# Kernel optimization log

Hardware: AMD Instinct MI355X
Metric: run time of the kernel (lower is better)

## Reference

```python
import jax, jax.numpy as jnp
import numpy as np
from jax.scipy.linalg import solve_triangular

REG = 1e-6  # reg_covar added to covariance diagonal
LOG2PI = float(np.log(2.0 * np.pi))
RESP_EPS = 10.0 * float(np.finfo(np.float32).eps)


def _log_gauss(X, means, covs):
    # X: [N,D], means: [K,D], covs: [K,D,D] -> per-sample per-component log N(x|mu_k, Sigma_k): [N,K]
    K, D = means.shape
    eye = jnp.eye(D, dtype=X.dtype)
    chol = jnp.linalg.cholesky(covs + REG * eye)                      # [K,D,D]
    diff = X[None, :, :] - means[:, None, :]                          # [K,N,D]
    sol = jax.vmap(lambda L, d: solve_triangular(L, d.T, lower=True))(chol, diff)  # [K,D,N]
    maha = jnp.sum(sol * sol, axis=1)                                 # [K,N]
    logdet = jnp.sum(jnp.log(jnp.diagonal(chol, axis1=1, axis2=2)), axis=1)  # [K] = 0.5*log|Sigma|
    return (-0.5 * (D * LOG2PI + maha) - logdet[:, None]).T           # [N,K]


def _em_step(X, weights, means, covs):
    N, D = X.shape
    # E-step: responsibilities via stable logsumexp
    lp = _log_gauss(X, means, covs) + jnp.log(weights)[None, :]       # [N,K]
    log_norm = jax.scipy.special.logsumexp(lp, axis=1)                # [N]
    resp = jnp.exp(lp - log_norm[:, None])                            # [N,K]
    # M-step (MLE)
    nk = resp.sum(axis=0) + RESP_EPS                                  # [K]
    new_w = nk / N
    new_means = (resp.T @ X) / nk[:, None]                            # [K,D]
    diff = X[None, :, :] - new_means[:, None, :]                      # [K,N,D]
    new_covs = jnp.einsum('kn,knd,kne->kde', resp.T, diff, diff) / nk[:, None, None]
    new_covs = new_covs + REG * jnp.eye(D, dtype=X.dtype)
    return new_w, new_means, new_covs


def reference(X, weights, means, covariances, n_iter):
    # Normalize provided weights (uniform init in the torch module)
    w0 = weights / jnp.sum(weights)

    def step(carry, _):
        w, m, c = carry
        return _em_step(X, w, m, c), None

    (w, m, c), _ = jax.lax.scan(step, (w0, means, covariances), xs=None, length=n_iter)
    # Final per-sample log-likelihood under the fitted mixture (lower bound)
    lp = _log_gauss(X, m, c) + jnp.log(w)[None, :]
    return jax.scipy.special.logsumexp(lp, axis=1)                    # [N]


def setup_inputs() -> dict:
    key = jax.random.key(0)
    kx, km = jax.random.split(key)
    N, D, K = 100000, 32, 16
    X = jax.random.normal(kx, (N, D), dtype=jnp.float32)
    weights = jnp.ones((K,), dtype=jnp.float32) / K
    means = jax.random.normal(km, (K, D), dtype=jnp.float32)
    covariances = jnp.tile(jnp.eye(D, dtype=jnp.float32)[None], (K, 1, 1))
    return {"X": X, "weights": weights, "means": means, "covariances": covariances, "n_iter": 5}
```

## Files before the change

kernel.cpp:

```cpp
#include <hip/hip_runtime.h>
#include <math.h>

#define REGC 1e-6f
#define LOG2PI 1.83787706640934534f
#define RESP_EPS 1.1920929e-6f

#define NSLOT 64
#define SSTR 568

typedef __attribute__((ext_vector_type(8))) short short8;
typedef __attribute__((ext_vector_type(4))) float f32x4;
typedef unsigned short ushort_t;
typedef unsigned int uint_t;

__device__ __forceinline__ ushort_t f2bf(float x) {
    uint_t u = __float_as_uint(x);
    uint_t r = (u + 0x7fffu + ((u >> 16) & 1u)) >> 16;
    return (ushort_t)r;
}
__device__ __forceinline__ float bf2f(ushort_t h) {
    return __uint_as_float(((uint_t)h) << 16);
}
__device__ __forceinline__ f32x4 shx4(f32x4 v, int m) {
    f32x4 r;
#pragma unroll
    for (int i = 0; i < 4; ++i) r[i] = __shfl_xor(v[i], m);
    return r;
}
__device__ __forceinline__ f32x4 sel4(bool s, f32x4 b, f32x4 a) {
    f32x4 r;
#pragma unroll
    for (int i = 0; i < 4; ++i) r[i] = s ? b[i] : a[i];
    return r;
}
__device__ __forceinline__ short8 pack_rx(const float* r8, const short8 bh, float& row) {
    uint_t u[8];
#pragma unroll
    for (int jj = 0; jj < 8; ++jj) {
        float av = r8[jj] * bf2f((ushort_t)bh[jj]);
        row += av;
        u[jj] = __float_as_uint(av) + 0x8000u;
    }
    short8 out;
    uint_t* o = (uint_t*)&out;
    o[0] = __builtin_amdgcn_perm(u[1], u[0], 0x07060302);
    o[1] = __builtin_amdgcn_perm(u[3], u[2], 0x07060302);
    o[2] = __builtin_amdgcn_perm(u[5], u[4], 0x07060302);
    o[3] = __builtin_amdgcn_perm(u[7], u[6], 0x07060302);
    return out;
}

__global__ __launch_bounds__(256) void gmm_prep(const float* __restrict__ X,
                                                const float* __restrict__ w,
                                                const float* __restrict__ mu,
                                                const float* __restrict__ cov,
                                                ushort_t* __restrict__ Xh,
                                                ushort_t* __restrict__ Xl,
                                                ushort_t* __restrict__ XTH,
                                                ushort_t* __restrict__ Wh,
                                                ushort_t* __restrict__ Wl,
                                                float* __restrict__ Bv,
                                                float* __restrict__ Cc,
                                                float* __restrict__ S,
                                                int* __restrict__ cnt,
                                                int N, int NCB) {
    int t = threadIdx.x;
    if ((int)blockIdx.x < NCB) {
        int chunk = blockIdx.x;
        __shared__ float xsh[32][33];
        int s = t >> 3, q = t & 7;
        int n = chunk * 32 + s;
        float4 v = make_float4(0.f, 0.f, 0.f, 0.f);
        if (n < N) v = ((const float4*)(X + (size_t)n * 32))[q];
        float vv[4] = { v.x, v.y, v.z, v.w };
        xsh[s][q * 4 + 0] = v.x; xsh[s][q * 4 + 1] = v.y;
        xsh[s][q * 4 + 2] = v.z; xsh[s][q * 4 + 3] = v.w;
        if (n < N) {
            ushort_t h[4], l[4];
#pragma unroll
            for (int i = 0; i < 4; ++i) {
                h[i] = f2bf(vv[i]);
                l[i] = f2bf(vv[i] - bf2f(h[i]));
            }
            size_t o = (size_t)n * 32 + q * 4;
            *(uint2*)(Xh + o) = make_uint2((uint_t)h[0] | ((uint_t)h[1] << 16),
                                           (uint_t)h[2] | ((uint_t)h[3] << 16));
            *(uint2*)(Xl + o) = make_uint2((uint_t)l[0] | ((uint_t)l[1] << 16),
                                           (uint_t)l[2] | ((uint_t)l[3] << 16));
        }
        __syncthreads();
        int di = t >> 7;
        int lane = (t >> 1) & 63;
        int jj0 = (t & 1) * 4;
        int c = lane & 15, quad = lane >> 4;
        int d = di * 16 + c;
        ushort_t fh[4];
#pragma unroll
        for (int i = 0; i < 4; ++i) fh[i] = f2bf(xsh[quad * 8 + jj0 + i][d]);
        size_t fo = ((size_t)(chunk * 2 + di) * 64 + lane) * 8 + jj0;
        *(uint2*)(XTH + fo) = make_uint2((uint_t)fh[0] | ((uint_t)fh[1] << 16),
                                         (uint_t)fh[2] | ((uint_t)fh[3] << 16));
        return;
    }
    int k = (int)blockIdx.x - NCB;
    __shared__ float L[32][33];
    __shared__ float Ai[32][33];
    if (t >= 64) {
        for (int idx = t - 64; idx < NSLOT * SSTR; idx += 192)
            S[(size_t)k * NSLOT * SSTR + idx] = 0.f;
        if (k == 0 && t - 64 < 8) cnt[t - 64] = 0;
        return;
    }
    const float* cv = cov + (size_t)k * 1024;
    const float* muk = mu + (size_t)k * 32;
#pragma unroll
    for (int rep = 0; rep < 16; ++rep) {
        int idx = rep * 64 + t;
        int i = idx >> 5, j = idx & 31;
        L[i][j] = cv[idx] + (i == j ? REGC : 0.f);
    }
    asm volatile("" ::: "memory");
#pragma unroll
    for (int j = 0; j < 32; ++j) {
        float s = L[j][j];
#pragma unroll
        for (int p = 0; p < j; ++p) { float v = L[j][p]; s -= v * v; }
        float dj = sqrtf(s);
        if (t > j && t < 32) {
            float s2 = L[t][j];
#pragma unroll
            for (int p = 0; p < j; ++p) s2 -= L[t][p] * L[j][p];
            L[t][j] = s2 / dj;
        }
        if (t == j) L[j][j] = dj;
        asm volatile("" ::: "memory");
    }
    if (t < 32) {
        float ai[32];
#pragma unroll
        for (int r = 0; r < 32; ++r) {
            float s = (r == t) ? 1.f : 0.f;
#pragma unroll
            for (int p = 0; p < r; ++p) s -= L[r][p] * ai[p];
            ai[r] = s / L[r][r];
        }
#pragma unroll
        for (int r = 0; r < 32; ++r) Ai[r][t] = ai[r];
    }
    asm volatile("" ::: "memory");
#pragma unroll
    for (int rep = 0; rep < 16; ++rep) {
        int idx = rep * 64 + t;
        int i = idx >> 5, j = idx & 31;
        float v = Ai[i][j];
        ushort_t h = f2bf(v);
        Wh[(size_t)(k * 32 + i) * 32 + j] = h;
        Wl[(size_t)(k * 32 + i) * 32 + j] = f2bf(v - bf2f(h));
    }
    if (t < 32) {
        float s = 0.f;
#pragma unroll
        for (int j = 0; j < 32; ++j) s += Ai[t][j] * muk[j];
        Bv[k * 32 + t] = s;
    }
    float wsum = 0.f;
#pragma unroll
    for (int i = 0; i < 16; ++i) wsum += w[i];
    float lv = (t < 32) ? logf(L[t & 31][t & 31]) : 0.f;
#pragma unroll
    for (int off = 1; off < 32; off <<= 1) lv += __shfl_xor(lv, off);
    if (t == 0) Cc[k] = logf(w[k] / wsum) - 0.5f * 32.0f * LOG2PI - lv;
}

__global__ __launch_bounds__(512) __attribute__((amdgpu_waves_per_eu(4)))
void gmm_emstep(const ushort_t* __restrict__ Xh, const ushort_t* __restrict__ Xl,
                const ushort_t* __restrict__ XTH,
                ushort_t* __restrict__ Wh, ushort_t* __restrict__ Wl,
                float* __restrict__ Bv, float* __restrict__ Cc,
                float* __restrict__ S, int* __restrict__ cnt,
                int N, int MB, int it) {
    __shared__ float rsh[16][260];
    int t = threadIdx.x;
    int wave = t >> 6, lane = t & 63;
    int quad = lane >> 4, c = lane & 15;
    int bid = (int)blockIdx.x;

    int wstart0 = bid * 256 + wave * 32;
    bool dup = (wstart0 + 32 > N);
    int wst = dup ? ((N >= 32) ? N - 32 : 0) : wstart0;

    size_t xo0 = (size_t)(wst + c) * 32 + quad * 8;
    size_t xo1 = (size_t)(wst + 16 + c) * 32 + quad * 8;
    short8 ah0 = *(const short8*)(Xh + xo0);
    short8 al0 = *(const short8*)(Xl + xo0);
    short8 ah1 = *(const short8*)(Xh + xo1);
    short8 al1 = *(const short8*)(Xl + xo1);

    {
        f32x4 p0[2], p1[2], p2[2], p3[2], fin[2];
#pragma unroll
        for (int k = 0; k < 16; ++k) {
            size_t w0 = (size_t)(k * 32 + c) * 32 + quad * 8;
            size_t w1 = w0 + 512;
            short8 bh0 = *(const short8*)(Wh + w0);
            short8 bl0 = *(const short8*)(Wl + w0);
            short8 bh1 = *(const short8*)(Wh + w1);
            short8 bl1 = *(const short8*)(Wl + w1);
            float bv0 = Bv[k * 32 + c];
            float bv1 = Bv[k * 32 + 16 + c];
#pragma unroll
            for (int tt = 0; tt < 2; ++tt) {
                short8 ah = tt ? ah1 : ah0;
                short8 al = tt ? al1 : al0;
                f32x4 a0 = {0.f, 0.f, 0.f, 0.f};
                f32x4 a1 = {0.f, 0.f, 0.f, 0.f};
                a0 = __builtin_amdgcn_mfma_f32_16x16x32_bf16(ah, bh0, a0, 0, 0, 0);
                a0 = __builtin_amdgcn_mfma_f32_16x16x32_bf16(ah, bl0, a0, 0, 0, 0);
                a0 = __builtin_amdgcn_mfma_f32_16x16x32_bf16(al, bh0, a0, 0, 0, 0);
                a1 = __builtin_amdgcn_mfma_f32_16x16x32_bf16(ah, bh1, a1, 0, 0, 0);
                a1 = __builtin_amdgcn_mfma_f32_16x16x32_bf16(ah, bl1, a1, 0, 0, 0);
                a1 = __builtin_amdgcn_mfma_f32_16x16x32_bf16(al, bh1, a1, 0, 0, 0);
                f32x4 ms;
#pragma unroll
                for (int r = 0; r < 4; ++r) {
                    float d0 = a0[r] - bv0;
                    float d1 = a1[r] - bv1;
                    ms[r] = fmaf(d0, d0, d1 * d1);
                }
                if ((k & 1) == 0) { p0[tt] = ms; }
                else {
                    f32x4 a = p0[tt] + shx4(p0[tt], 1);
                    f32x4 b = ms + shx4(ms, 1);
                    f32x4 v = sel4((c & 1) != 0, b, a);
                    if ((k & 2) == 0) { p1[tt] = v; }
                    else {
                        a = p1[tt] + shx4(p1[tt], 2); b = v + shx4(v, 2); v = sel4((c & 2) != 0, b, a);
                        if ((k & 4) == 0) { p2[tt] = v; }
                        else {
                            a = p2[tt] + shx4(p2[tt], 4); b = v + shx4(v, 4); v = sel4((c & 4) != 0, b, a);
                            if ((k & 8) == 0) { p3[tt] = v; }
                            else {
                                a = p3[tt] + shx4(p3[tt], 8); b = v + shx4(v, 8);
                                fin[tt] = sel4((c & 8) != 0, b, a);
                            }
                        }
                    }
                }
            }
        }
        float ccv = Cc[c];
#pragma unroll
        for (int tt = 0; tt < 2; ++tt) {
            f32x4 lp;
#pragma unroll
            for (int r = 0; r < 4; ++r) lp[r] = ccv - 0.5f * fin[tt][r];
            f32x4 mx = lp;
#pragma unroll
            for (int off = 1; off < 16; off <<= 1) {
                f32x4 s = shx4(mx, off);
#pragma unroll
                for (int r = 0; r < 4; ++r) mx[r] = fmaxf(mx[r], s[r]);
            }
            f32x4 e;
#pragma unroll
            for (int r = 0; r < 4; ++r) e[r] = __expf(lp[r] - mx[r]);
            f32x4 sm = e;
#pragma unroll
            for (int off = 1; off < 16; off <<= 1) sm = sm + shx4(sm, off);
            f32x4 sv;
#pragma unroll
            for (int r = 0; r < 4; ++r) sv[r] = dup ? 0.f : e[r] / sm[r];
            *(f32x4*)&rsh[c][wave * 32 + tt * 16 + quad * 4] = sv;
        }
    }
    __syncthreads();

    {
        int slot = bid & (NSLOT - 1);
        f32x4 q00[2], q01[2], q11[2];
#pragma unroll
        for (int kk = 0; kk < 2; ++kk) {
            q00[kk] = (f32x4){0.f, 0.f, 0.f, 0.f};
            q01[kk] = (f32x4){0.f, 0.f, 0.f, 0.f};
            q11[kk] = (f32x4){0.f, 0.f, 0.f, 0.f};
        }
        float row0[2] = {0.f, 0.f}, row1[2] = {0.f, 0.f}, corner[2] = {0.f, 0.f};

#pragma unroll 2
        for (int ch = 0; ch < 8; ++ch) {
            size_t fb = (((size_t)(bid * 8 + ch)) * 128 + lane) * 8;
            short8 bh0 = *(const short8*)(XTH + fb);
            short8 bh1 = *(const short8*)(XTH + fb + 512);
#pragma unroll
            for (int kk = 0; kk < 2; ++kk) {
                int k = wave + kk * 8;
                float r8[8];
#pragma unroll
                for (int jj = 0; jj < 8; ++jj) r8[jj] = rsh[k][ch * 32 + quad * 8 + jj];
                corner[kk] += ((r8[0] + r8[1]) + (r8[2] + r8[3])) +
                              ((r8[4] + r8[5]) + (r8[6] + r8[7]));
                short8 a0 = pack_rx(r8, bh0, row0[kk]);
                short8 a1 = pack_rx(r8, bh1, row1[kk]);
                q00[kk] = __builtin_amdgcn_mfma_f32_16x16x32_bf16(a0, bh0, q00[kk], 0, 0, 0);
                q01[kk] = __builtin_amdgcn_mfma_f32_16x16x32_bf16(a0, bh1, q01[kk], 0, 0, 0);
                q11[kk] = __builtin_amdgcn_mfma_f32_16x16x32_bf16(a1, bh1, q11[kk], 0, 0, 0);
            }
        }
#pragma unroll
        for (int kk = 0; kk < 2; ++kk) {
            row0[kk] += __shfl_xor(row0[kk], 16);  row0[kk] += __shfl_xor(row0[kk], 32);
            row1[kk] += __shfl_xor(row1[kk], 16);  row1[kk] += __shfl_xor(row1[kk], 32);
            corner[kk] += __shfl_xor(corner[kk], 16);  corner[kk] += __shfl_xor(corner[kk], 32);

            int k = wave + kk * 8;
            float* pb = S + ((size_t)(k * NSLOT + slot)) * SSTR;
#pragma unroll
            for (int r = 0; r < 4; ++r) {
                int i = quad * 4 + r;
                int base = i * 32 - ((i * (i + 1)) >> 1);
                if (c >= i) atomicAdd(&pb[base + c], q00[kk][r]);
                atomicAdd(&pb[base + 16 + c], q01[kk][r]);
                int i2 = 16 + i;
                if (c >= i) atomicAdd(&pb[i2 * 32 - ((i2 * (i2 + 1)) >> 1) + 16 + c],
                                      q11[kk][r]);
            }
            if (quad == 0) {
                atomicAdd(&pb[528 + c], row0[kk]);
                atomicAdd(&pb[528 + 16 + c], row1[kk]);
            }
            if (lane == 0) atomicAdd(&pb[560], corner[kk]);
        }
    }
    __syncthreads();
    if (t == 0) atomicAdd(&cnt[it], 1);

    if (bid >= 16) return;

    if (t == 0) {
        volatile int* vc = cnt + it;
        while (*vc < MB) __builtin_amdgcn_s_sleep(16);
    }
    __syncthreads();

    int k = bid;
    float* Ssh   = &rsh[0][0];
    float* Lsh   = Ssh + 576;
    float* Aish  = Lsh + 1056;
    float* meansh = Aish + 1056;

    for (int idx = t; idx < 561; idx += 512) {
        float s = 0.f;
        float* sp = S + (size_t)k * NSLOT * SSTR + idx;
#pragma unroll 8
        for (int b = 0; b < NSLOT; ++b) s += sp[(size_t)b * SSTR];
        Ssh[idx] = s;
#pragma unroll 8
        for (int b = 0; b < NSLOT; ++b) sp[(size_t)b * SSTR] = 0.f;
    }
    __syncthreads();
    float nk = Ssh[560] + RESP_EPS;
    float inv = 1.f / nk;
    if (t < 32) meansh[t] = Ssh[528 + t] * inv;
    __syncthreads();
#pragma unroll
    for (int i0 = 0; i0 < 2; ++i0) {
        int i = i0 * 16 + (t >> 5), j = t & 31;
        int a = i < j ? i : j;
        int b2 = i < j ? j : i;
        float cv = Ssh[a * 32 - ((a * (a + 1)) >> 1) + b2];
        Lsh[i * 33 + j] = cv * inv - meansh[i] * meansh[j] + ((i == j) ? 2.f * REGC : 0.f);
    }
    __syncthreads();
    if (t < 64) {
#pragma unroll
        for (int j = 0; j < 32; ++j) {
            float s = Lsh[j * 33 + j];
#pragma unroll
            for (int p = 0; p < j; ++p) { float v = Lsh[j * 33 + p]; s -= v * v; }
            float dj = sqrtf(s);
            if (t > j && t < 32) {
                float s2 = Lsh[t * 33 + j];
#pragma unroll
                for (int p = 0; p < j; ++p) s2 -= Lsh[t * 33 + p] * Lsh[j * 33 + p];
                Lsh[t * 33 + j] = s2 / dj;
            }
            if (t == j) Lsh[j * 33 + j] = dj;
            asm volatile("" ::: "memory");
        }
        if (t < 32) {
            float ai[32];
#pragma unroll
            for (int r = 0; r < 32; ++r) {
                float s = (r == t) ? 1.f : 0.f;
#pragma unroll
                for (int p = 0; p < r; ++p) s -= Lsh[r * 33 + p] * ai[p];
                ai[r] = s / Lsh[r * 33 + r];
            }
#pragma unroll
            for (int r = 0; r < 32; ++r) Aish[r * 33 + t] = ai[r];
        }
    }
    __syncthreads();
#pragma unroll
    for (int i0 = 0; i0 < 2; ++i0) {
        int i = i0 * 16 + (t >> 5), j = t & 31;
        float v = Aish[i * 33 + j];
        ushort_t h = f2bf(v);
        Wh[(size_t)(k * 32 + i) * 32 + j] = h;
        Wl[(size_t)(k * 32 + i) * 32 + j] = f2bf(v - bf2f(h));
    }
    if (t < 32) {
        float s = 0.f;
#pragma unroll
        for (int j = 0; j < 32; ++j) s += Aish[t * 33 + j] * meansh[j];
        Bv[k * 32 + t] = s;
    }
    float lv = (t < 32) ? logf(Lsh[(t & 31) * 33 + (t & 31)]) : 0.f;
#pragma unroll
    for (int off = 1; off < 32; off <<= 1) lv += __shfl_xor(lv, off);
    if (t == 0) Cc[k] = logf(nk / (float)N) - 0.5f * 32.0f * LOG2PI - lv;
}

__global__ __launch_bounds__(256, 2) void gmm_estep_fin(const ushort_t* __restrict__ Xh,
                                                        const ushort_t* __restrict__ Xl,
                                                        const ushort_t* __restrict__ Wh,
                                                        const ushort_t* __restrict__ Wl,
                                                        const float* __restrict__ Bv,
                                                        const float* __restrict__ Cc,
                                                        float* __restrict__ out,
                                                        int N) {
    int t = threadIdx.x;
    int wave = t >> 6, lane = t & 63;
    int quad = lane >> 4, c = lane & 15;
    int wstart = (blockIdx.x * 4 + wave) * 32;
    if (wstart + 32 > N) wstart = (N >= 32) ? (N - 32) : 0;
    bool al4 = ((N & 3) == 0);

    size_t xo0 = (size_t)(wstart + c) * 32 + quad * 8;
    size_t xo1 = (size_t)(wstart + 16 + c) * 32 + quad * 8;
    short8 ah0 = *(const short8*)(Xh + xo0);
    short8 al0 = *(const short8*)(Xl + xo0);
    short8 ah1 = *(const short8*)(Xh + xo1);
    short8 al1 = *(const short8*)(Xl + xo1);

    f32x4 p0[2], p1[2], p2[2], p3[2], fin[2];
#pragma unroll
    for (int k = 0; k < 16; ++k) {
        size_t w0 = (size_t)(k * 32 + c) * 32 + quad * 8;
        size_t w1 = w0 + 512;
        short8 bh0 = *(const short8*)(Wh + w0);
        short8 bl0 = *(const short8*)(Wl + w0);
        short8 bh1 = *(const short8*)(Wh + w1);
        short8 bl1 = *(const short8*)(Wl + w1);
        float bv0 = Bv[k * 32 + c];
        float bv1 = Bv[k * 32 + 16 + c];
#pragma unroll
        for (int tt = 0; tt < 2; ++tt) {
            short8 ah = tt ? ah1 : ah0;
            short8 al = tt ? al1 : al0;
            f32x4 a0 = {0.f, 0.f, 0.f, 0.f};
            f32x4 a1 = {0.f, 0.f, 0.f, 0.f};
            a0 = __builtin_amdgcn_mfma_f32_16x16x32_bf16(ah, bh0, a0, 0, 0, 0);
            a0 = __builtin_amdgcn_mfma_f32_16x16x32_bf16(ah, bl0, a0, 0, 0, 0);
            a0 = __builtin_amdgcn_mfma_f32_16x16x32_bf16(al, bh0, a0, 0, 0, 0);
            a1 = __builtin_amdgcn_mfma_f32_16x16x32_bf16(ah, bh1, a1, 0, 0, 0);
            a1 = __builtin_amdgcn_mfma_f32_16x16x32_bf16(ah, bl1, a1, 0, 0, 0);
            a1 = __builtin_amdgcn_mfma_f32_16x16x32_bf16(al, bh1, a1, 0, 0, 0);
            f32x4 ms;
#pragma unroll
            for (int r = 0; r < 4; ++r) {
                float d0 = a0[r] - bv0;
                float d1 = a1[r] - bv1;
                ms[r] = fmaf(d0, d0, d1 * d1);
            }
            if ((k & 1) == 0) { p0[tt] = ms; }
            else {
                f32x4 a = p0[tt] + shx4(p0[tt], 1);
                f32x4 b = ms + shx4(ms, 1);
                f32x4 v = sel4((c & 1) != 0, b, a);
                if ((k & 2) == 0) { p1[tt] = v; }
                else {
                    a = p1[tt] + shx4(p1[tt], 2); b = v + shx4(v, 2); v = sel4((c & 2) != 0, b, a);
                    if ((k & 4) == 0) { p2[tt] = v; }
                    else {
                        a = p2[tt] + shx4(p2[tt], 4); b = v + shx4(v, 4); v = sel4((c & 4) != 0, b, a);
                        if ((k & 8) == 0) { p3[tt] = v; }
                        else {
                            a = p3[tt] + shx4(p3[tt], 8); b = v + shx4(v, 8);
                            fin[tt] = sel4((c & 8) != 0, b, a);
                        }
                    }
                }
            }
        }
    }
    float ccv = Cc[c];
#pragma unroll
    for (int tt = 0; tt < 2; ++tt) {
        f32x4 lp;
#pragma unroll
        for (int r = 0; r < 4; ++r) lp[r] = ccv - 0.5f * fin[tt][r];
        f32x4 mx = lp;
#pragma unroll
        for (int off = 1; off < 16; off <<= 1) {
            f32x4 s = shx4(mx, off);
#pragma unroll
            for (int r = 0; r < 4; ++r) mx[r] = fmaxf(mx[r], s[r]);
        }
        f32x4 e;
#pragma unroll
        for (int r = 0; r < 4; ++r) e[r] = __expf(lp[r] - mx[r]);
        f32x4 sm = e;
#pragma unroll
        for (int off = 1; off < 16; off <<= 1) sm = sm + shx4(sm, off);
        if (c == 0) {
            int nb = wstart + tt * 16 + quad * 4;
            f32x4 o;
#pragma unroll
            for (int r = 0; r < 4; ++r) o[r] = mx[r] + __logf(sm[r]);
            if (al4) *(f32x4*)(out + nb) = o;
            else { for (int r = 0; r < 4; ++r) out[nb + r] = o[r]; }
        }
    }
}

extern "C" void kernel_launch(void* const* d_in, const int* in_sizes, int n_in,
                              void* d_out, int out_size, void* d_ws, size_t ws_size,
                              hipStream_t stream) {
    const float* X   = (const float*)d_in[0];
    const float* w   = (const float*)d_in[1];
    const float* mu  = (const float*)d_in[2];
    const float* cov = (const float*)d_in[3];
    const int NITER = 5;
    int N = in_sizes[0] / 32;
    int MB = (N + 255) / 256;
    int NCB = MB * 8;

    float* ws = (float*)d_ws;
    float*    Bv = ws;
    float*    Cc = ws + 512;
    ushort_t* Wh = (ushort_t*)(ws + 528);
    ushort_t* Wl = (ushort_t*)(ws + 8720);
    ushort_t* Xh = (ushort_t*)(ws + 16912);
    ushort_t* Xl = (ushort_t*)(ws + 16912 + (size_t)16 * N);
    size_t xt0 = 16912 + (size_t)32 * N;
    size_t XTHf = (size_t)NCB * 512;
    ushort_t* XTH = (ushort_t*)(ws + xt0);
    float*  S   = ws + xt0 + XTHf;
    int*    cnt = (int*)(S + (size_t)16 * NSLOT * SSTR);

    float* out = (float*)d_out;

    int eblocks = ((N + 31) / 32 + 3) / 4;

    gmm_prep<<<NCB + 16, 256, 0, stream>>>(X, w, mu, cov, Xh, Xl, XTH, Wh, Wl,
                                           Bv, Cc, S, cnt, N, NCB);

    for (int it = 0; it < NITER; ++it)
        gmm_emstep<<<MB, 512, 0, stream>>>(Xh, Xl, XTH, Wh, Wl, Bv, Cc, S, cnt,
                                           N, MB, it);

    gmm_estep_fin<<<eblocks, 256, 0, stream>>>(Xh, Xl, Wh, Wl, Bv, Cc, out, N);
}
```

Baseline: 507.7 us.

## Replace slot-based atomic accumulation with per-block partial stores and ordered counter

Each block now writes its per-component sufficient statistics to its own partial buffer with plain relaxed stores, replacing atomicAdd into 64 shared slots. The 16 finalizer blocks then sum over all MB blocks' partials, and the slot-zeroing passes in the prep kernel and the finalizer are gone. The completion counter now uses release/acquire atomics. This removes atomic contention on the accumulators, but each finalizer block must read about 391 partials per element instead of 64, so more serial reduction work lands on just 16 blocks.

```diff
diff --git a/kernel.cpp b/kernel.cpp
--- a/kernel.cpp
+++ b/kernel.cpp
@@ -5,13 +5,15 @@
 #define LOG2PI 1.83787706640934534f
 #define RESP_EPS 1.1920929e-6f
 
-#define NSLOT 64
-#define SSTR 568
+#define PART_K 561
 
 typedef __attribute__((ext_vector_type(8))) short short8;
 typedef __attribute__((ext_vector_type(4))) float f32x4;
 typedef unsigned short ushort_t;
 typedef unsigned int uint_t;
+
+#define STC(p, v) __hip_atomic_store((p), (v), __ATOMIC_RELAXED, __HIP_MEMORY_SCOPE_AGENT)
+#define LDC(p)    __hip_atomic_load((p), __ATOMIC_RELAXED, __HIP_MEMORY_SCOPE_AGENT)
 
 __device__ __forceinline__ ushort_t f2bf(float x) {
     uint_t u = __float_as_uint(x);
@@ -61,7 +63,6 @@
                                                 ushort_t* __restrict__ Wl,
                                                 float* __restrict__ Bv,
                                                 float* __restrict__ Cc,
-                                                float* __restrict__ S,
                                                 int* __restrict__ cnt,
                                                 int N, int NCB) {
     int t = threadIdx.x;
@@ -106,8 +107,6 @@
     __shared__ float L[32][33];
     __shared__ float Ai[32][33];
     if (t >= 64) {
-        for (int idx = t - 64; idx < NSLOT * SSTR; idx += 192)
-            S[(size_t)k * NSLOT * SSTR + idx] = 0.f;
         if (k == 0 && t - 64 < 8) cnt[t - 64] = 0;
         return;
     }
@@ -177,7 +176,7 @@
                 const ushort_t* __restrict__ XTH,
                 ushort_t* __restrict__ Wh, ushort_t* __restrict__ Wl,
                 float* __restrict__ Bv, float* __restrict__ Cc,
-                float* __restrict__ S, int* __restrict__ cnt,
+                float* __restrict__ part, int* __restrict__ cnt,
                 int N, int MB, int it) {
     __shared__ float rsh[16][260];
     int t = threadIdx.x;
@@ -276,7 +275,6 @@
     __syncthreads();
 
     {
-        int slot = bid & (NSLOT - 1);
         f32x4 q00[2], q01[2], q11[2];
 #pragma unroll
         for (int kk = 0; kk < 2; ++kk) {
@@ -313,32 +311,33 @@
             corner[kk] += __shfl_xor(corner[kk], 16);  corner[kk] += __shfl_xor(corner[kk], 32);
 
             int k = wave + kk * 8;
-            float* pb = S + ((size_t)(k * NSLOT + slot)) * SSTR;
+            float* pb = part + ((size_t)bid * 16 + k) * PART_K;
 #pragma unroll
             for (int r = 0; r < 4; ++r) {
                 int i = quad * 4 + r;
                 int base = i * 32 - ((i * (i + 1)) >> 1);
-                if (c >= i) atomicAdd(&pb[base + c], q00[kk][r]);
-                atomicAdd(&pb[base + 16 + c], q01[kk][r]);
+                if (c >= i) STC(&pb[base + c], q00[kk][r]);
+                STC(&pb[base + 16 + c], q01[kk][r]);
                 int i2 = 16 + i;
-                if (c >= i) atomicAdd(&pb[i2 * 32 - ((i2 * (i2 + 1)) >> 1) + 16 + c],
-                                      q11[kk][r]);
+                if (c >= i) STC(&pb[i2 * 32 - ((i2 * (i2 + 1)) >> 1) + 16 + c],
+                                q11[kk][r]);
             }
             if (quad == 0) {
-                atomicAdd(&pb[528 + c], row0[kk]);
-                atomicAdd(&pb[528 + 16 + c], row1[kk]);
-            }
-            if (lane == 0) atomicAdd(&pb[560], corner[kk]);
-        }
-    }
-    __syncthreads();
-    if (t == 0) atomicAdd(&cnt[it], 1);
+                STC(&pb[528 + c], row0[kk]);
+                STC(&pb[528 + 16 + c], row1[kk]);
+            }
+            if (lane == 0) STC(&pb[560], corner[kk]);
+        }
+    }
+    __syncthreads();
+    if (t == 0)
+        __hip_atomic_fetch_add(&cnt[it], 1, __ATOMIC_RELEASE, __HIP_MEMORY_SCOPE_AGENT);
 
     if (bid >= 16) return;
 
     if (t == 0) {
-        volatile int* vc = cnt + it;
-        while (*vc < MB) __builtin_amdgcn_s_sleep(16);
+        while (__hip_atomic_load(&cnt[it], __ATOMIC_ACQUIRE, __HIP_MEMORY_SCOPE_AGENT) < MB)
+            __builtin_amdgcn_s_sleep(8);
     }
     __syncthreads();
 
@@ -348,14 +347,13 @@
     float* Aish  = Lsh + 1056;
     float* meansh = Aish + 1056;
 
-    for (int idx = t; idx < 561; idx += 512) {
+    for (int idx = t; idx < PART_K; idx += 512) {
         float s = 0.f;
-        float* sp = S + (size_t)k * NSLOT * SSTR + idx;
-#pragma unroll 8
-        for (int b = 0; b < NSLOT; ++b) s += sp[(size_t)b * SSTR];
+        const float* sp = part + (size_t)k * PART_K + idx;
+#pragma unroll 4
+        for (int b = 0; b < MB; ++b)
+            s += LDC(sp + (size_t)b * 16 * PART_K);
         Ssh[idx] = s;
-#pragma unroll 8
-        for (int b = 0; b < NSLOT; ++b) sp[(size_t)b * SSTR] = 0.f;
     }
     __syncthreads();
     float nk = Ssh[560] + RESP_EPS;
@@ -546,18 +544,18 @@
     size_t xt0 = 16912 + (size_t)32 * N;
     size_t XTHf = (size_t)NCB * 512;
     ushort_t* XTH = (ushort_t*)(ws + xt0);
-    float*  S   = ws + xt0 + XTHf;
-    int*    cnt = (int*)(S + (size_t)16 * NSLOT * SSTR);
+    float*  part = ws + xt0 + XTHf;
+    int*    cnt  = (int*)(part + (size_t)MB * 16 * PART_K);
 
     float* out = (float*)d_out;
 
     int eblocks = ((N + 31) / 32 + 3) / 4;
 
     gmm_prep<<<NCB + 16, 256, 0, stream>>>(X, w, mu, cov, Xh, Xl, XTH, Wh, Wl,
-                                           Bv, Cc, S, cnt, N, NCB);
+                                           Bv, Cc, cnt, N, NCB);
 
     for (int it = 0; it < NITER; ++it)
-        gmm_emstep<<<MB, 512, 0, stream>>>(Xh, Xl, XTH, Wh, Wl, Bv, Cc, S, cnt,
+        gmm_emstep<<<MB, 512, 0, stream>>>(Xh, Xl, XTH, Wh, Wl, Bv, Cc, part, cnt,
                                            N, MB, it);
 
     gmm_estep_fin<<<eblocks, 256, 0, stream>>>(Xh, Xl, Wh, Wl, Bv, Cc, out, N);
```

Measured after the change: 761.1 us. 49.9% more time.
